# Kernel optimization log

Hardware: AMD Instinct MI355X
Metric: run time of the kernel (lower is better)

Reference implementation:

```python
import jax, jax.numpy as jnp
import numpy as np
from jax import lax

B = 2048                 # scenes = agent/av/env nodes
K_OTH, K_LANE = 16, 32
N_OTH, N_LANE = B * K_OTH, B * K_LANE
T_HIST, T_AV, T_PRED = 20, 20, 30
H = 25                   # LSTM hidden
NH, FO = 5, 5            # GAT heads / out feats


def _lstm(x, Wih, Whh, b, h0, c0):
    # x: [T, N, I]; torch gate order i, f, g, o
    def step(carry, xt):
        h, c = carry
        g = xt @ Wih.T + h @ Whh.T + b
        i, f, gg, o = jnp.split(g, 4, axis=-1)
        c = jax.nn.sigmoid(f) * c + jax.nn.sigmoid(i) * jnp.tanh(gg)
        h = jax.nn.sigmoid(o) * jnp.tanh(c)
        return (h, c), h
    (h, c), hs = lax.scan(step, (h0, c0), x)
    return hs, h, c


def _seg_mean(x, idx, n):
    s = jax.ops.segment_sum(x, idx, num_segments=n)
    cnt = jax.ops.segment_sum(jnp.ones((x.shape[0],), x.dtype), idx, num_segments=n)
    return s / cnt[:, None]


def _gat(src_feat, dst_feat, src_idx, dst_idx, W, al, ar, b, n_dst):
    # DGL GATConv: shared fc for src/dst, leaky_relu(0.2), edge-softmax per dst node/head
    fs = (src_feat @ W.T).reshape(-1, NH, FO)   # [Ns, NH, FO]
    fd = (dst_feat @ W.T).reshape(-1, NH, FO)   # [Nd, NH, FO]
    el = (fs * al).sum(-1)                      # [Ns, NH]
    er = (fd * ar).sum(-1)                      # [Nd, NH]
    e = jax.nn.leaky_relu(el[src_idx] + er[dst_idx], negative_slope=0.2)  # [E, NH]
    emax = jax.ops.segment_max(e, dst_idx, num_segments=n_dst)
    ee = jnp.exp(e - emax[dst_idx])
    a = ee / jax.ops.segment_sum(ee, dst_idx, num_segments=n_dst)[dst_idx]
    out = jax.ops.segment_sum(fs[src_idx] * a[:, :, None], dst_idx, num_segments=n_dst)
    return out + b.reshape(NH, FO)              # [Nd, NH, FO]


def setup_inputs():
    key = jax.random.key(0)
    ks = iter(jax.random.split(key, 48))
    def rn(shape, s=1.0):
        return jax.random.normal(next(ks), shape, jnp.float32) * s
    def lstm_p(pre, i):
        return {pre + '_Wih': rn((4 * H, i), 0.2), pre + '_Whh': rn((4 * H, H), 0.2), pre + '_b': rn((4 * H,), 0.1)}
    def gat_p(pre):
        return {pre + '_W': rn((NH * FO, H), 0.2), pre + '_al': rn((NH, FO), 0.2), pre + '_ar': rn((NH, FO), 0.2), pre + '_b': rn((NH * FO,), 0.1)}
    inp = {
        'agent_state': rn((B, T_HIST + T_PRED, 2)),
        'av_state': rn((B, T_AV, 2)),
        'others_state': rn((N_OTH, T_AV, 2)),
        'lane_state': rn((N_LANE, T_AV, 2)),
    }
    inp.update(lstm_p('ag', 2)); inp.update(lstm_p('av', 2)); inp.update(lstm_p('ot', 2)); inp.update(lstm_p('de', 1))
    inp['lin_W'] = rn((2, H), 0.2); inp['lin_b'] = rn((2,), 0.1)
    inp.update(gat_p('gav')); inp.update(gat_p('got')); inp.update(gat_p('gln'))
    inp['others_dst'] = jnp.arange(N_OTH, dtype=jnp.int32) // K_OTH   # env id of each 'others' node
    inp['lane_dst'] = jnp.arange(N_LANE, dtype=jnp.int32) // K_LANE   # env id of each 'lane' node
    return inp


def reference(agent_state, av_state, others_state, lane_state,
              ag_Wih, ag_Whh, ag_b, av_Wih, av_Whh, av_b, ot_Wih, ot_Whh, ot_b,
              de_Wih, de_Whh, de_b, lin_W, lin_b,
              gav_W, gav_al, gav_ar, gav_b, got_W, got_al, got_ar, got_b,
              gln_W, gln_al, gln_ar, gln_b, others_dst, lane_dst):
    Bn = agent_state.shape[0]
    dt = agent_state.dtype
    z = lambda n: jnp.zeros((n, H), dt)

    # --- LSTM encoders (time-major, like torch nn.LSTM) ---
    agent = jnp.transpose(agent_state[:, :T_HIST, :], (1, 0, 2))
    _, ag_h, ag_c = _lstm(agent, ag_Wih, ag_Whh, ag_b, z(Bn), z(Bn))
    _, _, av_c = _lstm(jnp.transpose(av_state, (1, 0, 2)), av_Wih, av_Whh, av_b, z(Bn), z(Bn))
    no, nl = others_state.shape[0], lane_state.shape[0]
    _, _, ot_c = _lstm(jnp.transpose(others_state, (1, 0, 2)), ot_Wih, ot_Whh, ot_b, z(no), z(no))
    # NOTE: original code encodes lanes with the *agent* encoder (faithful to source bug)
    _, _, ln_c = _lstm(jnp.transpose(lane_state, (1, 0, 2)), ag_Wih, ag_Whh, ag_b, z(nl), z(nl))

    # --- update_all(copy_u, mean) ---
    env_agent_info = ag_c                       # exactly one agent per env -> mean == identity
    env_lane_info = _seg_mean(ln_c, lane_dst, Bn)

    # --- HeteroGraphConv of 3 GATConvs, aggregate='mean' ---
    e_av = _gat(av_c, env_agent_info, jnp.arange(Bn), jnp.arange(Bn), gav_W, gav_al, gav_ar, gav_b, Bn)
    e_ot = _gat(ot_c, env_agent_info, jnp.arange(no), others_dst, got_W, got_al, got_ar, got_b, Bn)
    e_ln = _gat(ln_c, env_agent_info, jnp.arange(nl), lane_dst, gln_W, gln_al, gln_ar, gln_b, Bn)
    env_code = ((e_av + e_ot + e_ln) / 3.0).reshape(Bn, NH * FO)   # [B, 25]

    # --- LSTM decoder over t = arange(0, 3, 0.1) ---
    t = jnp.broadcast_to(jnp.arange(0.0, 3.0, 0.1, dtype=dt).reshape(T_PRED, 1, 1), (T_PRED, Bn, 1))
    hs, _, _ = _lstm(t, de_Wih, de_Whh, de_b, ag_h, ag_c + env_code)
    predict = jnp.transpose(hs @ lin_W.T + lin_b, (1, 0, 2))       # [B, 30, 2]
    return predict, env_lane_info
```

## Files before the change

kernel.cpp:

```cpp
#include <hip/hip_runtime.h>


typedef __attribute__((ext_vector_type(8))) short s16x8;
typedef __attribute__((ext_vector_type(4))) float fx4;

__device__ __forceinline__ float frcp(float x) { return __builtin_amdgcn_rcpf(x); }
__device__ __forceinline__ float fsig(float x) { return frcp(1.f + __expf(-x)); }
__device__ __forceinline__ float ftanh(float x) { return 1.f - 2.f * frcp(1.f + __expf(2.f * x)); }

__device__ __forceinline__ unsigned bfhi(float f) {
    unsigned b = __float_as_uint(f);
    return (b + 0x7FFFu + ((b >> 16) & 1u)) >> 16;
}
__device__ __forceinline__ float bfval(unsigned h) { return __uint_as_float(h << 16); }
__device__ __forceinline__ unsigned packsplit(float f) {
    unsigned h = bfhi(f);
    unsigned l = bfhi(f - bfval(h));
    return h | (l << 16);
}

struct BF { s16x8 hi, lo; };
__device__ __forceinline__ BF buildB(const unsigned* L, int q, int n) {
    unsigned rb[8];
#pragma unroll
    for (int e = 0; e < 8; ++e) rb[e] = L[(8 * q + e) * 17 + n];
    union { unsigned w[4]; s16x8 v; } H, Lo;
#pragma unroll
    for (int i = 0; i < 4; ++i) {
        H.w[i]  = __builtin_amdgcn_perm(rb[2 * i + 1], rb[2 * i], 0x05040100u);
        Lo.w[i] = __builtin_amdgcn_perm(rb[2 * i + 1], rb[2 * i], 0x07060302u);
    }
    BF r; r.hi = H.v; r.lo = Lo.v; return r;
}

__global__ __launch_bounds__(64, 1) void enc_kernel(
    const float* __restrict__ agent, const float* __restrict__ av,
    const float* __restrict__ oth,   const float* __restrict__ lane,
    const float* __restrict__ agWih, const float* __restrict__ agWhh, const float* __restrict__ agB,
    const float* __restrict__ avWih, const float* __restrict__ avWhh, const float* __restrict__ avB,
    const float* __restrict__ otWih, const float* __restrict__ otWhh, const float* __restrict__ otB,
    float* __restrict__ ws)
{
    __shared__ unsigned hlds[32 * 17];

    const int l   = threadIdx.x & 63;
    const int n   = l & 15;
    const int q   = l >> 4;
    unsigned* L = hlds;

    const int g0 = blockIdx.x;
    int task;
    if (g0 < 128) task = 0;
    else if (g0 < 256) task = 1;
    else if (g0 < 2304) task = 2;
    else task = 3;

    const float* Whh; const float* Wih; const float* Bp;
    if (task == 1)      { Wih = avWih; Whh = avWhh; Bp = avB; }
    else if (task == 2) { Wih = otWih; Whh = otWhh; Bp = otB; }
    else                { Wih = agWih; Whh = agWhh; Bp = agB; }

    const int node = g0 * 16 + n;
    const float* xp;
    if (task == 0)      xp = agent + node * 100;
    else if (task == 1) xp = av   + (node - 2048)  * 40;
    else if (task == 2) xp = oth  + (node - 4096)  * 40;
    else                xp = lane + (node - 36864) * 40;

    float xv[10];
#pragma unroll
    for (int s = 0; s < 5; ++s) {
        float2 t2 = *reinterpret_cast<const float2*>(xp + 2 * (5 * q + s));
        xv[2 * s] = t2.x; xv[2 * s + 1] = t2.y;
    }

    s16x8 Ahi[7], Alo[7];
#pragma unroll
    for (int T = 0; T < 7; ++T) {
        const int p = 16 * T + n;
        const int r = p & 3;
        const int u = p >> 2;
        int row = r * 25 + u;
        if (row > 99) row = 99;
        float w[8];
        if (q < 3) {
            const float* src = Whh + row * 25 + 8 * q;
#pragma unroll
            for (int e = 0; e < 8; ++e) w[e] = src[e];
        } else {
            w[0] = Whh[row * 25 + 24];
            w[1] = Wih[row * 2];
            w[2] = Wih[row * 2 + 1];
            w[3] = Bp[row];
            w[4] = w[5] = w[6] = w[7] = 0.f;
        }
#pragma unroll
        for (int e = 0; e < 8; ++e) {
            unsigned h = bfhi(w[e]);
            unsigned lo = bfhi(w[e] - bfval(h));
            Ahi[T][e] = (short)h;
            Alo[T][e] = (short)lo;
        }
    }

#pragma unroll
    for (int T = 0; T < 6; ++T) L[(4 * T + q) * 17 + n] = 0u;
    if (q == 0) {
        L[24 * 17 + n] = 0u;
        L[25 * 17 + n] = packsplit(xv[0]);
        L[26 * 17 + n] = packsplit(xv[1]);
    }
    if (q == 3) L[27 * 17 + n] = 0x00003F80u;
    L[(28 + q) * 17 + n] = 0u;
    __builtin_amdgcn_wave_barrier();

    BF Bf = buildB(L, q, n);

    float c[7], hv[7];
#pragma unroll
    for (int T = 0; T < 7; ++T) { c[T] = 0.f; hv[T] = 0.f; }

    const fx4 zero4 = {0.f, 0.f, 0.f, 0.f};

#pragma unroll 1
    for (int tt = 0; tt < 4; ++tt) {
#pragma unroll
        for (int s = 0; s < 5; ++s) {
            fx4 acc[7];
#pragma unroll
            for (int T = 0; T < 7; ++T) {
                fx4 a = __builtin_amdgcn_mfma_f32_16x16x32_bf16(Ahi[T], Bf.hi, zero4, 0, 0, 0);
                a = __builtin_amdgcn_mfma_f32_16x16x32_bf16(Ahi[T], Bf.lo, a, 0, 0, 0);
                a = __builtin_amdgcn_mfma_f32_16x16x32_bf16(Alo[T], Bf.hi, a, 0, 0, 0);
                acc[T] = a;
            }
#pragma unroll
            for (int T = 0; T < 7; ++T) {
                const float iv = fsig(acc[T][0]);
                const float fv = fsig(acc[T][1]);
                const float gv = ftanh(acc[T][2]);
                const float ov = fsig(acc[T][3]);
                c[T]  = fv * c[T] + iv * gv;
                hv[T] = ov * ftanh(c[T]);
            }
            const bool lastStep = (tt == 3) && (s == 4);
            if (!lastStep) {
#pragma unroll
                for (int T = 0; T < 6; ++T) L[(4 * T + q) * 17 + n] = packsplit(hv[T]);
                if (q == 0) L[24 * 17 + n] = packsplit(hv[6]);
                if (s < 4) {
                    if (q == tt) {
                        L[25 * 17 + n] = packsplit(xv[2 * (s + 1)]);
                        L[26 * 17 + n] = packsplit(xv[2 * (s + 1) + 1]);
                    }
                } else {
                    if (q == tt + 1) {
                        L[25 * 17 + n] = packsplit(xv[0]);
                        L[26 * 17 + n] = packsplit(xv[1]);
                    }
                }
                __builtin_amdgcn_wave_barrier();
                Bf = buildB(L, q, n);
            }
        }
    }

    float* dst_c; float* dst_h = nullptr;
    if (task == 0)      { dst_h = ws + node * 25; dst_c = ws + 51200 + node * 25; }
    else if (task == 1) dst_c = ws + 102400 + (node - 2048) * 25;
    else if (task == 2) dst_c = ws + 153600 + (node - 4096) * 25;
    else                dst_c = ws + 972800 + (node - 36864) * 25;
#pragma unroll
    for (int T = 0; T < 7; ++T) {
        const int u = 4 * T + q;
        if (u < 25) {
            dst_c[u] = c[T];
            if (task == 0) dst_h[u] = hv[T];
        }
    }
}

__global__ __launch_bounds__(256) void gat_kernel(
    const float* __restrict__ ws,
    const float* __restrict__ gavW, const float* __restrict__ gavAl, const float* __restrict__ gavAr, const float* __restrict__ gavB,
    const float* __restrict__ gotW, const float* __restrict__ gotAl, const float* __restrict__ gotAr, const float* __restrict__ gotB,
    const float* __restrict__ glnW, const float* __restrict__ glnAl, const float* __restrict__ glnAr, const float* __restrict__ glnB,
    float* __restrict__ envcode, float* __restrict__ lane_out)
{
    __shared__ float X[50 * 25];
    __shared__ float F[52 * 25];
    __shared__ float er[10];
    __shared__ float Eo[16 * 5];
    __shared__ float El[32 * 5];

    const int tid = threadIdx.x;
    const int b = blockIdx.x;
    const float* agc = ws + 51200;
    const float* avc = ws + 102400;
    const float* otc = ws + 153600;
    const float* lnc = ws + 972800;

    for (int i = tid; i < 1250; i += 256) {
        int r = i / 25, k = i - r * 25;
        float v;
        if (r == 0)      v = agc[b * 25 + k];
        else if (r == 1) v = avc[b * 25 + k];
        else if (r < 18) v = otc[(b * 16 + (r - 2)) * 25 + k];
        else             v = lnc[(b * 32 + (r - 18)) * 25 + k];
        X[i] = v;
    }
    __syncthreads();

    for (int d = tid; d < 1300; d += 256) {
        int row = d / 25, o = d - row * 25;
        const float* W; const float* xs;
        if (row == 0)      { W = gavW; xs = &X[1 * 25]; }
        else if (row == 1) { W = gavW; xs = &X[0]; }
        else if (row == 2) { W = gotW; xs = &X[0]; }
        else if (row == 3) { W = glnW; xs = &X[0]; }
        else if (row < 20) { W = gotW; xs = &X[(2 + row - 4) * 25]; }
        else               { W = glnW; xs = &X[(18 + row - 20) * 25]; }
        float acc = 0.f;
#pragma unroll
        for (int k = 0; k < 25; ++k) acc += W[o * 25 + k] * xs[k];
        F[row * 25 + o] = acc;
    }
    __syncthreads();

    if (tid < 10) {
        int conv = tid / 5, nn = tid - conv * 5;
        const float* ar = conv ? glnAr : gotAr;
        const float* fd = &F[(2 + conv) * 25];
        float acc = 0.f;
#pragma unroll
        for (int f = 0; f < 5; ++f) acc += fd[nn * 5 + f] * ar[nn * 5 + f];
        er[tid] = acc;
    }
    __syncthreads();

    for (int d = tid; d < 240; d += 256) {
        if (d < 80) {
            int i = d / 5, nn = d - i * 5;
            const float* fsrow = &F[(4 + i) * 25];
            float acc = er[nn];
#pragma unroll
            for (int f = 0; f < 5; ++f) acc += fsrow[nn * 5 + f] * gotAl[nn * 5 + f];
            Eo[d] = (acc > 0.f) ? acc : 0.2f * acc;
        } else {
            int d2 = d - 80;
            int i = d2 / 5, nn = d2 - i * 5;
            const float* fsrow = &F[(20 + i) * 25];
            float acc = er[5 + nn];
#pragma unroll
            for (int f = 0; f < 5; ++f) acc += fsrow[nn * 5 + f] * glnAl[nn * 5 + f];
            El[d2] = (acc > 0.f) ? acc : 0.2f * acc;
        }
    }
    __syncthreads();

    if (tid < 10) {
        int conv = tid / 5, nn = tid - conv * 5;
        if (conv == 0) {
            float m = -1e30f;
            for (int i = 0; i < 16; ++i) m = fmaxf(m, Eo[i * 5 + nn]);
            float s = 0.f;
            for (int i = 0; i < 16; ++i) s += __expf(Eo[i * 5 + nn] - m);
            float inv = frcp(s);
            for (int i = 0; i < 16; ++i) Eo[i * 5 + nn] = __expf(Eo[i * 5 + nn] - m) * inv;
        } else {
            float m = -1e30f;
            for (int i = 0; i < 32; ++i) m = fmaxf(m, El[i * 5 + nn]);
            float s = 0.f;
            for (int i = 0; i < 32; ++i) s += __expf(El[i * 5 + nn] - m);
            float inv = frcp(s);
            for (int i = 0; i < 32; ++i) El[i * 5 + nn] = __expf(El[i * 5 + nn] - m) * inv;
        }
    }
    __syncthreads();

    if (tid < 25) {
        const int o = tid, nn = o / 5;
        float v_av = F[o] + gavB[o];
        float s = 0.f;
        for (int i = 0; i < 16; ++i) s += Eo[i * 5 + nn] * F[(4 + i) * 25 + o];
        float v_ot = s + gotB[o];
        s = 0.f;
        for (int i = 0; i < 32; ++i) s += El[i * 5 + nn] * F[(20 + i) * 25 + o];
        float v_ln = s + glnB[o];
        envcode[b * 25 + o] = (v_av + v_ot + v_ln) * (1.f / 3.f);
        float m = 0.f;
        for (int i = 0; i < 32; ++i) m += X[(18 + i) * 25 + o];
        lane_out[b * 25 + o] = m * (1.f / 32.f);
    }
}

__global__ __launch_bounds__(256) void dec_kernel(
    const float* __restrict__ ws,
    const float* __restrict__ deWih, const float* __restrict__ deWhh, const float* __restrict__ deB,
    const float* __restrict__ linW,  const float* __restrict__ linB,
    float* __restrict__ out)
{
    __shared__ float hbuf[8][28];
    const int tid  = threadIdx.x;
    const int lane = tid & 63;
    const int half = lane >> 5;
    const int u    = lane & 31;
    const int u2   = (u < 25) ? u : 0;
    const bool act = (u < 25);
    const int wglob = (blockIdx.x * 256 + tid) >> 6;
    const int b = wglob * 2 + half;
    const int envloc = ((tid >> 6) << 1) + half;

    float U[4][25], Wi[4], Bb[4];
#pragma unroll
    for (int r = 0; r < 4; ++r) {
        const int row = u2 + 25 * r;
#pragma unroll
        for (int k = 0; k < 25; ++k) U[r][k] = deWhh[row * 25 + k];
        Wi[r] = deWih[row];
        Bb[r] = deB[row];
    }
    const int j = u & 1;
    float lw[25];
#pragma unroll
    for (int k = 0; k < 25; ++k) lw[k] = linW[j * 25 + k];
    const float lb = linB[j];

    const float* agh = ws;
    const float* agc = ws + 51200;
    const float* env = ws + 2611200;

    float h[25];
#pragma unroll
    for (int k = 0; k < 25; ++k) h[k] = agh[b * 25 + k];
    float c_own = agc[b * 25 + u2] + env[b * 25 + u2];

    for (int t = 0; t < 30; ++t) {
        const float tt = 0.1f * (float)t;
        float g[4];
#pragma unroll
        for (int r = 0; r < 4; ++r) {
            float acc = Bb[r] + Wi[r] * tt;
#pragma unroll
            for (int k = 0; k < 25; ++k) acc += U[r][k] * h[k];
            g[r] = acc;
        }
        const float iv = fsig(g[0]);
        const float fv = fsig(g[1]);
        const float gv = ftanh(g[2]);
        const float ov = fsig(g[3]);
        c_own = fv * c_own + iv * gv;
        const float ho = ov * ftanh(c_own);
        if (act) hbuf[envloc][u] = ho;
        __builtin_amdgcn_wave_barrier();
#pragma unroll
        for (int k = 0; k < 25; ++k) h[k] = hbuf[envloc][k];
        float ov2 = lb;
#pragma unroll
        for (int k = 0; k < 25; ++k) ov2 += lw[k] * h[k];
        if (u < 2) out[b * 60 + t * 2 + u] = ov2;
    }
}

extern "C" void kernel_launch(void* const* d_in, const int* in_sizes, int n_in,
                              void* d_out, int out_size, void* d_ws, size_t ws_size,
                              hipStream_t stream)
{
    const float* agent = (const float*)d_in[0];
    const float* av    = (const float*)d_in[1];
    const float* oth   = (const float*)d_in[2];
    const float* lane  = (const float*)d_in[3];
    const float* agWih = (const float*)d_in[4];
    const float* agWhh = (const float*)d_in[5];
    const float* agB   = (const float*)d_in[6];
    const float* avWih = (const float*)d_in[7];
    const float* avWhh = (const float*)d_in[8];
    const float* avB   = (const float*)d_in[9];
    const float* otWih = (const float*)d_in[10];
    const float* otWhh = (const float*)d_in[11];
    const float* otB   = (const float*)d_in[12];
    const float* deWih = (const float*)d_in[13];
    const float* deWhh = (const float*)d_in[14];
    const float* deB   = (const float*)d_in[15];
    const float* linW  = (const float*)d_in[16];
    const float* linB  = (const float*)d_in[17];
    const float* gavW  = (const float*)d_in[18];
    const float* gavAl = (const float*)d_in[19];
    const float* gavAr = (const float*)d_in[20];
    const float* gavB  = (const float*)d_in[21];
    const float* gotW  = (const float*)d_in[22];
    const float* gotAl = (const float*)d_in[23];
    const float* gotAr = (const float*)d_in[24];
    const float* gotB  = (const float*)d_in[25];
    const float* glnW  = (const float*)d_in[26];
    const float* glnAl = (const float*)d_in[27];
    const float* glnAr = (const float*)d_in[28];
    const float* glnB  = (const float*)d_in[29];

    float* out = (float*)d_out;
    float* ws  = (float*)d_ws;

    enc_kernel<<<6400, 64, 0, stream>>>(agent, av, oth, lane,
                                        agWih, agWhh, agB,
                                        avWih, avWhh, avB,
                                        otWih, otWhh, otB, ws);

    gat_kernel<<<2048, 256, 0, stream>>>(ws,
                                         gavW, gavAl, gavAr, gavB,
                                         gotW, gotAl, gotAr, gotB,
                                         glnW, glnAl, glnAr, glnB,
                                         ws + 2611200, out + 122880);

    dec_kernel<<<256, 256, 0, stream>>>(ws, deWih, deWhh, deB, linW, linB, out);
}
```

Before: 152.3 us.

## Process two node groups per encoder wave and fold exp scaling into weights

Each encoder wave now runs two independent 16-node LSTM groups, with their MFMA chains and gate math interleaved, so the grid is halved. The goal is to hide MFMA and transcendental latency in the serial recurrence and to share the A-fragment registers between both groups. The log2(e) factors are folded into the weights so gates use raw v_exp_f32. Hidden state is now stored as fp32 in LDS and split into bf16 hi/lo with v_cvt_pk_bf16_f32 when the B operand is built. This raises register pressure, and the task boundaries must fall on even block pairs.

```diff
diff --git a/kernel.cpp b/kernel.cpp
--- a/kernel.cpp
+++ b/kernel.cpp
@@ -8,29 +8,33 @@
 __device__ __forceinline__ float fsig(float x) { return frcp(1.f + __expf(-x)); }
 __device__ __forceinline__ float ftanh(float x) { return 1.f - 2.f * frcp(1.f + __expf(2.f * x)); }
 
+__device__ __forceinline__ float exp2p(float x) { float r; asm("v_exp_f32 %0, %1"  : "=v"(r) : "v"(x)); return r; }
+__device__ __forceinline__ float exp2m(float x) { float r; asm("v_exp_f32 %0, -%1" : "=v"(r) : "v"(x)); return r; }
+__device__ __forceinline__ float sigE(float gp)  { return frcp(1.f + exp2m(gp)); }
+__device__ __forceinline__ float tanhE(float gp) { return 1.f - 2.f * frcp(1.f + exp2p(gp)); }
+
 __device__ __forceinline__ unsigned bfhi(float f) {
     unsigned b = __float_as_uint(f);
     return (b + 0x7FFFu + ((b >> 16) & 1u)) >> 16;
 }
 __device__ __forceinline__ float bfval(unsigned h) { return __uint_as_float(h << 16); }
-__device__ __forceinline__ unsigned packsplit(float f) {
-    unsigned h = bfhi(f);
-    unsigned l = bfhi(f - bfval(h));
-    return h | (l << 16);
-}
-
-struct BF { s16x8 hi, lo; };
-__device__ __forceinline__ BF buildB(const unsigned* L, int q, int n) {
-    unsigned rb[8];
-#pragma unroll
-    for (int e = 0; e < 8; ++e) rb[e] = L[(8 * q + e) * 17 + n];
+
+__device__ __forceinline__ void buildB2(const float* L, int q, int n, s16x8& hi, s16x8& lo) {
+    float f[8];
+#pragma unroll
+    for (int e = 0; e < 8; ++e) f[e] = L[(8 * q + e) * 17 + n];
     union { unsigned w[4]; s16x8 v; } H, Lo;
 #pragma unroll
     for (int i = 0; i < 4; ++i) {
-        H.w[i]  = __builtin_amdgcn_perm(rb[2 * i + 1], rb[2 * i], 0x05040100u);
-        Lo.w[i] = __builtin_amdgcn_perm(rb[2 * i + 1], rb[2 * i], 0x07060302u);
-    }
-    BF r; r.hi = H.v; r.lo = Lo.v; return r;
+        unsigned hw;
+        asm("v_cvt_pk_bf16_f32 %0, %1, %2" : "=v"(hw) : "v"(f[2 * i]), "v"(f[2 * i + 1]));
+        const float r0 = f[2 * i]     - __uint_as_float(hw << 16);
+        const float r1 = f[2 * i + 1] - __uint_as_float(hw & 0xFFFF0000u);
+        unsigned lw;
+        asm("v_cvt_pk_bf16_f32 %0, %1, %2" : "=v"(lw) : "v"(r0), "v"(r1));
+        H.w[i] = hw; Lo.w[i] = lw;
+    }
+    hi = H.v; lo = Lo.v;
 }
 
 __global__ __launch_bounds__(64, 1) void enc_kernel(
@@ -41,18 +45,19 @@
     const float* __restrict__ otWih, const float* __restrict__ otWhh, const float* __restrict__ otB,
     float* __restrict__ ws)
 {
-    __shared__ unsigned hlds[32 * 17];
-
-    const int l   = threadIdx.x & 63;
-    const int n   = l & 15;
-    const int q   = l >> 4;
-    unsigned* L = hlds;
-
-    const int g0 = blockIdx.x;
+    __shared__ float hlds[2][32 * 17];
+
+    const int l = threadIdx.x & 63;
+    const int n = l & 15;
+    const int q = l >> 4;
+    float* LA = hlds[0];
+    float* LB = hlds[1];
+
+    const int gA = blockIdx.x * 2;
     int task;
-    if (g0 < 128) task = 0;
-    else if (g0 < 256) task = 1;
-    else if (g0 < 2304) task = 2;
+    if (gA < 128) task = 0;
+    else if (gA < 256) task = 1;
+    else if (gA < 2304) task = 2;
     else task = 3;
 
     const float* Whh; const float* Wih; const float* Bp;
@@ -60,20 +65,24 @@
     else if (task == 2) { Wih = otWih; Whh = otWhh; Bp = otB; }
     else                { Wih = agWih; Whh = agWhh; Bp = agB; }
 
-    const int node = g0 * 16 + n;
-    const float* xp;
-    if (task == 0)      xp = agent + node * 100;
-    else if (task == 1) xp = av   + (node - 2048)  * 40;
-    else if (task == 2) xp = oth  + (node - 4096)  * 40;
-    else                xp = lane + (node - 36864) * 40;
-
-    float xv[10];
+    const int nodeA = gA * 16 + n;
+    const int nodeB = nodeA + 16;
+    const float* xpA; const float* xpB;
+    if (task == 0)      { xpA = agent + nodeA * 100;          xpB = agent + nodeB * 100; }
+    else if (task == 1) { xpA = av + (nodeA - 2048) * 40;     xpB = av + (nodeB - 2048) * 40; }
+    else if (task == 2) { xpA = oth + (nodeA - 4096) * 40;    xpB = oth + (nodeB - 4096) * 40; }
+    else                { xpA = lane + (nodeA - 36864) * 40;  xpB = lane + (nodeB - 36864) * 40; }
+
+    float xvA[10], xvB[10];
 #pragma unroll
     for (int s = 0; s < 5; ++s) {
-        float2 t2 = *reinterpret_cast<const float2*>(xp + 2 * (5 * q + s));
-        xv[2 * s] = t2.x; xv[2 * s + 1] = t2.y;
-    }
-
+        float2 a2 = *reinterpret_cast<const float2*>(xpA + 2 * (5 * q + s));
+        float2 b2 = *reinterpret_cast<const float2*>(xpB + 2 * (5 * q + s));
+        xvA[2 * s] = a2.x; xvA[2 * s + 1] = a2.y;
+        xvB[2 * s] = b2.x; xvB[2 * s + 1] = b2.y;
+    }
+
+    const float L2E = 1.4426950408889634f;
     s16x8 Ahi[7], Alo[7];
 #pragma unroll
     for (int T = 0; T < 7; ++T) {
@@ -82,16 +91,17 @@
         const int u = p >> 2;
         int row = r * 25 + u;
         if (row > 99) row = 99;
+        const float sc = (r == 2) ? 2.f * L2E : L2E;
         float w[8];
         if (q < 3) {
             const float* src = Whh + row * 25 + 8 * q;
 #pragma unroll
-            for (int e = 0; e < 8; ++e) w[e] = src[e];
+            for (int e = 0; e < 8; ++e) w[e] = src[e] * sc;
         } else {
-            w[0] = Whh[row * 25 + 24];
-            w[1] = Wih[row * 2];
-            w[2] = Wih[row * 2 + 1];
-            w[3] = Bp[row];
+            w[0] = Whh[row * 25 + 24] * sc;
+            w[1] = Wih[row * 2] * sc;
+            w[2] = Wih[row * 2 + 1] * sc;
+            w[3] = Bp[row] * sc;
             w[4] = w[5] = w[6] = w[7] = 0.f;
         }
 #pragma unroll
@@ -104,78 +114,99 @@
     }
 
 #pragma unroll
-    for (int T = 0; T < 6; ++T) L[(4 * T + q) * 17 + n] = 0u;
+    for (int T = 0; T < 6; ++T) { LA[(4 * T + q) * 17 + n] = 0.f; LB[(4 * T + q) * 17 + n] = 0.f; }
     if (q == 0) {
-        L[24 * 17 + n] = 0u;
-        L[25 * 17 + n] = packsplit(xv[0]);
-        L[26 * 17 + n] = packsplit(xv[1]);
-    }
-    if (q == 3) L[27 * 17 + n] = 0x00003F80u;
-    L[(28 + q) * 17 + n] = 0u;
+        LA[24 * 17 + n] = 0.f;        LB[24 * 17 + n] = 0.f;
+        LA[25 * 17 + n] = xvA[0];     LB[25 * 17 + n] = xvB[0];
+        LA[26 * 17 + n] = xvA[1];     LB[26 * 17 + n] = xvB[1];
+    }
+    if (q == 3) { LA[27 * 17 + n] = 1.f; LB[27 * 17 + n] = 1.f; }
+    LA[(28 + q) * 17 + n] = 0.f; LB[(28 + q) * 17 + n] = 0.f;
     __builtin_amdgcn_wave_barrier();
 
-    BF Bf = buildB(L, q, n);
-
-    float c[7], hv[7];
-#pragma unroll
-    for (int T = 0; T < 7; ++T) { c[T] = 0.f; hv[T] = 0.f; }
+    s16x8 BhA, BlA, BhB, BlB;
+    buildB2(LA, q, n, BhA, BlA);
+    buildB2(LB, q, n, BhB, BlB);
+
+    float cA[7], hA[7], cB[7], hB[7];
+#pragma unroll
+    for (int T = 0; T < 7; ++T) { cA[T] = 0.f; hA[T] = 0.f; cB[T] = 0.f; hB[T] = 0.f; }
 
     const fx4 zero4 = {0.f, 0.f, 0.f, 0.f};
+    const float TL2E = 2.f * L2E;
 
 #pragma unroll 1
     for (int tt = 0; tt < 4; ++tt) {
 #pragma unroll
         for (int s = 0; s < 5; ++s) {
-            fx4 acc[7];
+            fx4 accA[7], accB[7];
 #pragma unroll
             for (int T = 0; T < 7; ++T) {
-                fx4 a = __builtin_amdgcn_mfma_f32_16x16x32_bf16(Ahi[T], Bf.hi, zero4, 0, 0, 0);
-                a = __builtin_amdgcn_mfma_f32_16x16x32_bf16(Ahi[T], Bf.lo, a, 0, 0, 0);
-                a = __builtin_amdgcn_mfma_f32_16x16x32_bf16(Alo[T], Bf.hi, a, 0, 0, 0);
-                acc[T] = a;
+                fx4 a = __builtin_amdgcn_mfma_f32_16x16x32_bf16(Ahi[T], BhA, zero4, 0, 0, 0);
+                a = __builtin_amdgcn_mfma_f32_16x16x32_bf16(Ahi[T], BlA, a, 0, 0, 0);
+                accA[T] = __builtin_amdgcn_mfma_f32_16x16x32_bf16(Alo[T], BhA, a, 0, 0, 0);
+                fx4 b = __builtin_amdgcn_mfma_f32_16x16x32_bf16(Ahi[T], BhB, zero4, 0, 0, 0);
+                b = __builtin_amdgcn_mfma_f32_16x16x32_bf16(Ahi[T], BlB, b, 0, 0, 0);
+                accB[T] = __builtin_amdgcn_mfma_f32_16x16x32_bf16(Alo[T], BhB, b, 0, 0, 0);
             }
 #pragma unroll
             for (int T = 0; T < 7; ++T) {
-                const float iv = fsig(acc[T][0]);
-                const float fv = fsig(acc[T][1]);
-                const float gv = ftanh(acc[T][2]);
-                const float ov = fsig(acc[T][3]);
-                c[T]  = fv * c[T] + iv * gv;
-                hv[T] = ov * ftanh(c[T]);
+                const float iv = sigE(accA[T][0]);
+                const float fv = sigE(accA[T][1]);
+                const float gv = tanhE(accA[T][2]);
+                const float ov = sigE(accA[T][3]);
+                cA[T] = fv * cA[T] + iv * gv;
+                hA[T] = ov * tanhE(cA[T] * TL2E);
+            }
+#pragma unroll
+            for (int T = 0; T < 7; ++T) {
+                const float iv = sigE(accB[T][0]);
+                const float fv = sigE(accB[T][1]);
+                const float gv = tanhE(accB[T][2]);
+                const float ov = sigE(accB[T][3]);
+                cB[T] = fv * cB[T] + iv * gv;
+                hB[T] = ov * tanhE(cB[T] * TL2E);
             }
             const bool lastStep = (tt == 3) && (s == 4);
             if (!lastStep) {
 #pragma unroll
-                for (int T = 0; T < 6; ++T) L[(4 * T + q) * 17 + n] = packsplit(hv[T]);
-                if (q == 0) L[24 * 17 + n] = packsplit(hv[6]);
+                for (int T = 0; T < 6; ++T) {
+                    LA[(4 * T + q) * 17 + n] = hA[T];
+                    LB[(4 * T + q) * 17 + n] = hB[T];
+                }
+                if (q == 0) { LA[24 * 17 + n] = hA[6]; LB[24 * 17 + n] = hB[6]; }
                 if (s < 4) {
                     if (q == tt) {
-                        L[25 * 17 + n] = packsplit(xv[2 * (s + 1)]);
-                        L[26 * 17 + n] = packsplit(xv[2 * (s + 1) + 1]);
+                        LA[25 * 17 + n] = xvA[2 * (s + 1)]; LA[26 * 17 + n] = xvA[2 * (s + 1) + 1];
+                        LB[25 * 17 + n] = xvB[2 * (s + 1)]; LB[26 * 17 + n] = xvB[2 * (s + 1) + 1];
                     }
                 } else {
                     if (q == tt + 1) {
-                        L[25 * 17 + n] = packsplit(xv[0]);
-                        L[26 * 17 + n] = packsplit(xv[1]);
+                        LA[25 * 17 + n] = xvA[0]; LA[26 * 17 + n] = xvA[1];
+                        LB[25 * 17 + n] = xvB[0]; LB[26 * 17 + n] = xvB[1];
                     }
                 }
                 __builtin_amdgcn_wave_barrier();
-                Bf = buildB(L, q, n);
+                buildB2(LA, q, n, BhA, BlA);
+                buildB2(LB, q, n, BhB, BlB);
             }
         }
     }
 
-    float* dst_c; float* dst_h = nullptr;
-    if (task == 0)      { dst_h = ws + node * 25; dst_c = ws + 51200 + node * 25; }
-    else if (task == 1) dst_c = ws + 102400 + (node - 2048) * 25;
-    else if (task == 2) dst_c = ws + 153600 + (node - 4096) * 25;
-    else                dst_c = ws + 972800 + (node - 36864) * 25;
+    float* dstcA; float* dsthA = nullptr;
+    float* dstcB; float* dsthB = nullptr;
+    if (task == 0)      { dsthA = ws + nodeA * 25; dstcA = ws + 51200 + nodeA * 25;
+                          dsthB = ws + nodeB * 25; dstcB = ws + 51200 + nodeB * 25; }
+    else if (task == 1) { dstcA = ws + 102400 + (nodeA - 2048) * 25;  dstcB = ws + 102400 + (nodeB - 2048) * 25; }
+    else if (task == 2) { dstcA = ws + 153600 + (nodeA - 4096) * 25;  dstcB = ws + 153600 + (nodeB - 4096) * 25; }
+    else                { dstcA = ws + 972800 + (nodeA - 36864) * 25; dstcB = ws + 972800 + (nodeB - 36864) * 25; }
 #pragma unroll
     for (int T = 0; T < 7; ++T) {
         const int u = 4 * T + q;
         if (u < 25) {
-            dst_c[u] = c[T];
-            if (task == 0) dst_h[u] = hv[T];
+            dstcA[u] = cA[T];
+            dstcB[u] = cB[T];
+            if (task == 0) { dsthA[u] = hA[T]; dsthB[u] = hB[T]; }
         }
     }
 }
@@ -400,7 +431,7 @@
     float* out = (float*)d_out;
     float* ws  = (float*)d_ws;
 
-    enc_kernel<<<6400, 64, 0, stream>>>(agent, av, oth, lane,
+    enc_kernel<<<3200, 64, 0, stream>>>(agent, av, oth, lane,
                                         agWih, agWhh, agB,
                                         avWih, avWhh, avB,
                                         otWih, otWhh, otB, ws);
```

Result: faster. 143.3 us (-5.9%).
